# Kernel tuning notes

Measured on AMD Instinct MI355X. Metric: run time of the kernel, lower is better.

The kernel has to match this reference:

```python
import jax, jax.numpy as jnp
import numpy as np

# DeformConv3d hyperparams (from init_kwargs)
STRIDE = (1, 1, 1)
PAD = (1, 1, 1)
DIL = (1, 1, 1)
GROUPS = 1
DEFORM_GROUPS = 1  # reference assumes dg == 1


def setup_inputs() -> dict:
    key = jax.random.key(0)
    k1, k2, k3, k4 = jax.random.split(key, 4)
    x = jax.random.normal(k1, (2, 32, 24, 24, 24), jnp.float32)
    # offset channels = 3 * dg * kD*kH*kW = 81, layout [k_idx, (dz,dy,dx)]
    offset = jax.random.normal(k2, (2, 81, 24, 24, 24), jnp.float32)
    weight = jax.random.normal(k3, (64, 32, 3, 3, 3), jnp.float32) * 0.05
    bias = jax.random.normal(k4, (64,), jnp.float32) * 0.05
    return {"x": x, "offset": offset, "weight": weight, "bias": bias}


def _deform_conv3d(x, offset, weight, bias):
    B, C, D, H, W = x.shape
    Cout, Cg, kD, kH, kW = weight.shape
    sD, sH, sW = STRIDE
    pD, pH, pW = PAD
    dD, dH, dW = DIL
    Kn = kD * kH * kW
    Do = (D + 2 * pD - dD * (kD - 1) - 1) // sD + 1
    Ho = (H + 2 * pH - dH * (kH - 1) - 1) // sH + 1
    Wo = (W + 2 * pW - dW * (kW - 1) - 1) // sW + 1
    N = Do * Ho * Wo

    # offset: [B, Kn*3, Do,Ho,Wo] -> [B, Kn, 3, N]
    off = offset.reshape(B, Kn, 3, N)

    # kernel tap grid [Kn]
    kz, ky, kx = jnp.meshgrid(jnp.arange(kD), jnp.arange(kH), jnp.arange(kW), indexing='ij')
    kz, ky, kx = kz.reshape(Kn), ky.reshape(Kn), kx.reshape(Kn)
    # output grid [N]
    oz, oy, ox = jnp.meshgrid(jnp.arange(Do), jnp.arange(Ho), jnp.arange(Wo), indexing='ij')
    oz, oy, ox = oz.reshape(N), oy.reshape(N), ox.reshape(N)

    # sampling coords [B, Kn, N]
    z = (oz[None, None, :] * sD - pD) + kz[None, :, None] * dD + off[:, :, 0]
    y = (oy[None, None, :] * sH - pH) + ky[None, :, None] * dH + off[:, :, 1]
    xx = (ox[None, None, :] * sW - pW) + kx[None, :, None] * dW + off[:, :, 2]

    z0 = jnp.floor(z); fz = z - z0
    y0 = jnp.floor(y); fy = y - y0
    x0 = jnp.floor(xx); fx = xx - x0

    x_flat = x.reshape(B, C, D * H * W)
    acc = jnp.zeros((B, C, Kn * N), x.dtype)
    # 8 trilinear corners (fixed small loop)
    for dz in (0, 1):
        iz = z0 + dz
        wz = fz if dz else (1.0 - fz)
        for dy in (0, 1):
            iy = y0 + dy
            wy = fy if dy else (1.0 - fy)
            for dx in (0, 1):
                ix = x0 + dx
                wx = fx if dx else (1.0 - fx)
                valid = ((iz >= 0) & (iz < D) & (iy >= 0) & (iy < H)
                         & (ix >= 0) & (ix < W))
                w = (wz * wy * wx) * valid.astype(x.dtype)  # [B,Kn,N]
                izc = jnp.clip(iz, 0, D - 1).astype(jnp.int32)
                iyc = jnp.clip(iy, 0, H - 1).astype(jnp.int32)
                ixc = jnp.clip(ix, 0, W - 1).astype(jnp.int32)
                idx = (izc * H + iyc) * W + ixc  # [B,Kn,N]
                g = jnp.take_along_axis(x_flat, idx.reshape(B, 1, Kn * N), axis=2)
                acc = acc + g * w.reshape(B, 1, Kn * N)

    # im2col columns ordered (c, kz, ky, kx) to match weight layout
    cols = acc.reshape(B, C * Kn, N)
    Cpg = C // GROUPS
    Opg = Cout // GROUPS
    cols_g = cols.reshape(B, GROUPS, Cpg * Kn, N)
    w_g = weight.reshape(GROUPS, Opg, Cpg * Kn)
    out = jnp.einsum('gok,bgkn->bgon', w_g, cols_g).reshape(B, Cout, N)
    out = out + bias[None, :, None]
    return out.reshape(B, Cout, Do, Ho, Wo)


def reference(x, offset, weight, bias):
    return _deform_conv3d(x, offset, weight, bias)
```

## Files before the change

kernel.cpp:

```cpp
#include <hip/hip_runtime.h>
#include <hip/hip_fp16.h>


constexpr int B   = 2;
constexpr int C   = 32;
constexpr int D   = 24, H = 24, W = 24;
constexpr int CO  = 64;
constexpr int KN  = 27;
constexpr int DHW = D * H * W;
constexpr int N   = DHW;
constexpr int CK  = C * KN;

constexpr int NPOS     = 32;
constexpr int NTAP     = NPOS * KN;
constexpr int NTASK    = NTAP * 4;
constexpr int TPB_MAIN = 576;
constexpr int PADR     = CK + 8;
constexpr int NBLK     = (B * N) / NPOS;

constexpr int PREPX_BLKS = (B * DHW) / 256;
constexpr int PREPW_BLKS = (CO * CK) / 256;

using h8v   = __attribute__((ext_vector_type(8))) _Float16;
using f32x4 = __attribute__((ext_vector_type(4))) float;

__device__ __forceinline__ h8v splat8(float w) {
    const _Float16 h = (_Float16)w;
    h8v r;
    #pragma unroll
    for (int i = 0; i < 8; ++i) r[i] = h;
    return r;
}

__device__ __forceinline__ unsigned pack2h(float a, float b) {
    const _Float16 ha = (_Float16)a, hb = (_Float16)b;
    unsigned short ua, ub;
    __builtin_memcpy(&ua, &ha, 2);
    __builtin_memcpy(&ub, &hb, 2);
    return (unsigned)ua | ((unsigned)ub << 16);
}

__global__ __launch_bounds__(256)
void prep_fused(const float* __restrict__ x, const float* __restrict__ wgt,
                _Float16* __restrict__ xT, _Float16* __restrict__ wp) {
    const int bid = blockIdx.x;
    if (bid < PREPX_BLKS) {
        __shared__ unsigned s_t[256 * 21];
        const int tid = threadIdx.x;
        const int v0  = bid * 256;
        const int b   = (v0 >= DHW) ? 1 : 0;
        const int vox = (v0 - b * DHW) + tid;
        const float* xb = x + (size_t)(b * C) * DHW + vox;
        #pragma unroll
        for (int c2 = 0; c2 < 16; ++c2) {
            const float f0 = xb[(size_t)(2 * c2)     * DHW];
            const float f1 = xb[(size_t)(2 * c2 + 1) * DHW];
            s_t[tid * 21 + c2] = pack2h(f0, f1);
        }
        __syncthreads();
        unsigned r[16];
        #pragma unroll
        for (int j = 0; j < 16; ++j) r[j] = s_t[tid * 21 + j];
        int4* dst = reinterpret_cast<int4*>(xT + ((size_t)(v0 + tid)) * 32);
        dst[0] = make_int4(r[0],  r[1],  r[2],  r[3]);
        dst[1] = make_int4(r[4],  r[5],  r[6],  r[7]);
        dst[2] = make_int4(r[8],  r[9],  r[10], r[11]);
        dst[3] = make_int4(r[12], r[13], r[14], r[15]);
    } else {
        const int idx   = (bid - PREPX_BLKS) * 256 + threadIdx.x;
        const int j     = idx & 7;
        const int lane  = (idx >> 3) & 63;
        const int t     = idx >> 9;
        const int otile = t / 27;
        const int kstep = t - otile * 27;
        const int o     = otile * 16 + (lane & 15);
        const int c     = 8 * (lane >> 4) + j;
        wp[idx] = (_Float16)wgt[(size_t)o * CK + c * KN + kstep];
    }
}

__global__ __launch_bounds__(TPB_MAIN, 5)
void deform_main(const float* __restrict__ off,
                 const _Float16* __restrict__ xT,
                 const _Float16* __restrict__ wp,
                 const float* __restrict__ bias,
                 float* __restrict__ out) {
    __shared__ _Float16 s_vb[NPOS * PADR];

    const int tid   = threadIdx.x;
    const int blk   = blockIdx.x;
    const int n0    = blk * NPOS;
    const int b     = n0 / N;
    const int nbase = n0 - b * N;
    const h8v* xbase = reinterpret_cast<const h8v*>(xT) + (size_t)b * DHW * 4;
    const float* offb = off + (size_t)(b * 81) * N;

    #pragma unroll 1
    for (int r = 0; r < 6; ++r) {
        const int tau = tid + r * TPB_MAIN;
        const int q   = tau & 3;
        const int tap = tau >> 2;
        const int p   = tap & 31;
        const int k   = tap >> 5;
        const int n   = nbase + p;
        const int oz = n / 576;
        const int rr = n - oz * 576;
        const int oy = rr / 24;
        const int ox = rr - oy * 24;
        const int kz = k / 9;
        const int kr = k - kz * 9;
        const int ky = kr / 3;
        const int kx = kr - ky * 3;

        const float offz = offb[((size_t)(k * 3 + 0)) * N + n];
        const float offy = offb[((size_t)(k * 3 + 1)) * N + n];
        const float offx = offb[((size_t)(k * 3 + 2)) * N + n];

        const float z  = (float)(oz - 1 + kz) + offz;
        const float y  = (float)(oy - 1 + ky) + offy;
        const float xx = (float)(ox - 1 + kx) + offx;
        const float zf = floorf(z), yf = floorf(y), xf = floorf(xx);
        const float fz = z - zf, fy = y - yf, fx = xx - xf;
        const int z0 = (int)zf, y0 = (int)yf, x0 = (int)xf;

        int   cidx[8];
        float cw[8];
        #pragma unroll
        for (int cr = 0; cr < 8; ++cr) {
            const int cz = cr >> 2, cy = (cr >> 1) & 1, cx = cr & 1;
            const int iz = z0 + cz, iy = y0 + cy, ix = x0 + cx;
            const bool vd = ((unsigned)iz < (unsigned)D) &&
                            ((unsigned)iy < (unsigned)H) &&
                            ((unsigned)ix < (unsigned)W);
            const int izc = min(max(iz, 0), D - 1);
            const int iyc = min(max(iy, 0), H - 1);
            const int ixc = min(max(ix, 0), W - 1);
            cidx[cr] = (izc * H + iyc) * W + ixc;
            const float wz = cz ? fz : 1.0f - fz;
            const float wy = cy ? fy : 1.0f - fy;
            const float wx = cx ? fx : 1.0f - fx;
            cw[cr] = vd ? (wz * wy * wx) : 0.0f;
        }

        h8v v[8];
        #pragma unroll
        for (int cr = 0; cr < 8; ++cr)
            v[cr] = xbase[(size_t)cidx[cr] * 4 + q];
        h8v acc = splat8(0.0f);
        #pragma unroll
        for (int cr = 0; cr < 8; ++cr)
            acc += v[cr] * splat8(cw[cr]);

        *reinterpret_cast<h8v*>(&s_vb[p * PADR + k * 32 + q * 8]) = acc;
    }
    __syncthreads();

    const int wv = tid >> 6;
    if (wv < 8) {
        const int lane = tid & 63;
        const int ot   = wv & 3;
        const int pt   = wv >> 2;
        const int p    = pt * 16 + (lane & 15);
        f32x4 acc4 = {0.f, 0.f, 0.f, 0.f};
        const h8v* wrow = reinterpret_cast<const h8v*>(wp) + (ot * 27) * 64 + lane;
        const int lrow = p * PADR;
        const int lcol = (lane >> 4) * 8;
        #pragma unroll
        for (int ks = 0; ks < 27; ++ks) {
            const h8v a  = wrow[ks * 64];
            const h8v bf = *reinterpret_cast<const h8v*>(&s_vb[lrow + ks * 32 + lcol]);
            acc4 = __builtin_amdgcn_mfma_f32_16x16x32_f16(a, bf, acc4, 0, 0, 0);
        }
        const int n = nbase + p;
        const int obase = ot * 16 + (lane >> 4) * 4;
        #pragma unroll
        for (int rr = 0; rr < 4; ++rr) {
            const int o = obase + rr;
            out[((size_t)(b * CO + o)) * N + n] = acc4[rr] + bias[o];
        }
    }
}

extern "C" void kernel_launch(void* const* d_in, const int* in_sizes, int n_in,
                              void* d_out, int out_size, void* d_ws, size_t ws_size,
                              hipStream_t stream) {
    const float* x    = (const float*)d_in[0];
    const float* off  = (const float*)d_in[1];
    const float* wgt  = (const float*)d_in[2];
    const float* bias = (const float*)d_in[3];
    float* out = (float*)d_out;

    _Float16* xT = (_Float16*)d_ws;
    _Float16* wp = (_Float16*)((char*)d_ws + 1769472);

    prep_fused<<<PREPX_BLKS + PREPW_BLKS, 256, 0, stream>>>(x, wgt, xT, wp);
    deform_main<<<NBLK, TPB_MAIN, 0, stream>>>(off, xT, wp, bias, out);
}
```

Before: 100.1 us.

## Fuse trilinear gather directly into MFMA fragments, removing LDS staging

Each wave now owns 16 output positions and, for each of the 27 taps, builds the B fragment for the MFMA in registers from the trilinear gather, then multiplies it against four weight tiles covering all 64 output channels. This removes the shared-memory im2col buffer, the block barrier, and the idle waves in the GEMM phase, and raises occupancy by dropping LDS use. In exchange, every wave reloads weight fragments from global memory for each tap, and the gather for a position is done by 4 lanes per wave instead of being spread over a larger block.

```diff
diff --git a/kernel.cpp b/kernel.cpp
--- a/kernel.cpp
+++ b/kernel.cpp
@@ -11,12 +11,8 @@
 constexpr int N   = DHW;
 constexpr int CK  = C * KN;
 
-constexpr int NPOS     = 32;
-constexpr int NTAP     = NPOS * KN;
-constexpr int NTASK    = NTAP * 4;
-constexpr int TPB_MAIN = 576;
-constexpr int PADR     = CK + 8;
-constexpr int NBLK     = (B * N) / NPOS;
+constexpr int TPB_MAIN = 256;
+constexpr int NBLK     = (B * N) / 64;
 
 constexpr int PREPX_BLKS = (B * DHW) / 256;
 constexpr int PREPW_BLKS = (CO * CK) / 256;
@@ -79,42 +75,49 @@
     }
 }
 
-__global__ __launch_bounds__(TPB_MAIN, 5)
+__global__ __launch_bounds__(TPB_MAIN)
 void deform_main(const float* __restrict__ off,
                  const _Float16* __restrict__ xT,
                  const _Float16* __restrict__ wp,
                  const float* __restrict__ bias,
                  float* __restrict__ out) {
-    __shared__ _Float16 s_vb[NPOS * PADR];
+    const int tid  = threadIdx.x;
+    const int lane = tid & 63;
+    const int wv   = tid >> 6;
+    const int p    = lane & 15;
+    const int q    = lane >> 4;
 
-    const int tid   = threadIdx.x;
-    const int blk   = blockIdx.x;
-    const int n0    = blk * NPOS;
-    const int b     = n0 / N;
-    const int nbase = n0 - b * N;
-    const h8v* xbase = reinterpret_cast<const h8v*>(xT) + (size_t)b * DHW * 4;
-    const float* offb = off + (size_t)(b * 81) * N;
+    const int gp = blockIdx.x * 64 + wv * 16 + p;
+    const int b  = (gp >= N) ? 1 : 0;
+    const int n  = gp - b * N;
+    const int oz = n / 576;
+    const int rr = n - oz * 576;
+    const int oy = rr / 24;
+    const int ox = rr - oy * 24;
+
+    const float* offb  = off + (size_t)(b * 81) * N + n;
+    const h8v*   xbase = reinterpret_cast<const h8v*>(xT) + (size_t)b * DHW * 4;
+    const h8v*   wbase = reinterpret_cast<const h8v*>(wp);
+
+    f32x4 acc[4];
+    #pragma unroll
+    for (int ot = 0; ot < 4; ++ot) acc[ot] = (f32x4){0.f, 0.f, 0.f, 0.f};
 
     #pragma unroll 1
-    for (int r = 0; r < 6; ++r) {
-        const int tau = tid + r * TPB_MAIN;
-        const int q   = tau & 3;
-        const int tap = tau >> 2;
-        const int p   = tap & 31;
-        const int k   = tap >> 5;
-        const int n   = nbase + p;
-        const int oz = n / 576;
-        const int rr = n - oz * 576;
-        const int oy = rr / 24;
-        const int ox = rr - oy * 24;
-        const int kz = k / 9;
-        const int kr = k - kz * 9;
+    for (int ks = 0; ks < KN; ++ks) {
+        const int kz = ks / 9;
+        const int kr = ks - kz * 9;
         const int ky = kr / 3;
         const int kx = kr - ky * 3;
 
-        const float offz = offb[((size_t)(k * 3 + 0)) * N + n];
-        const float offy = offb[((size_t)(k * 3 + 1)) * N + n];
-        const float offx = offb[((size_t)(k * 3 + 2)) * N + n];
+        const float offz = offb[(size_t)(ks * 3 + 0) * N];
+        const float offy = offb[(size_t)(ks * 3 + 1) * N];
+        const float offx = offb[(size_t)(ks * 3 + 2) * N];
+
+        h8v afr[4];
+        #pragma unroll
+        for (int ot = 0; ot < 4; ++ot)
+            afr[ot] = wbase[(ot * 27 + ks) * 64 + lane];
 
         const float z  = (float)(oz - 1 + kz) + offz;
         const float y  = (float)(oy - 1 + ky) + offy;
@@ -146,37 +149,24 @@
         #pragma unroll
         for (int cr = 0; cr < 8; ++cr)
             v[cr] = xbase[(size_t)cidx[cr] * 4 + q];
-        h8v acc = splat8(0.0f);
+
+        h8v bfr = splat8(0.0f);
         #pragma unroll
         for (int cr = 0; cr < 8; ++cr)
-            acc += v[cr] * splat8(cw[cr]);
+            bfr += v[cr] * splat8(cw[cr]);
 
-        *reinterpret_cast<h8v*>(&s_vb[p * PADR + k * 32 + q * 8]) = acc;
+        #pragma unroll
+        for (int ot = 0; ot < 4; ++ot)
+            acc[ot] = __builtin_amdgcn_mfma_f32_16x16x32_f16(afr[ot], bfr,
+                                                             acc[ot], 0, 0, 0);
     }
-    __syncthreads();
 
-    const int wv = tid >> 6;
-    if (wv < 8) {
-        const int lane = tid & 63;
-        const int ot   = wv & 3;
-        const int pt   = wv >> 2;
-        const int p    = pt * 16 + (lane & 15);
-        f32x4 acc4 = {0.f, 0.f, 0.f, 0.f};
-        const h8v* wrow = reinterpret_cast<const h8v*>(wp) + (ot * 27) * 64 + lane;
-        const int lrow = p * PADR;
-        const int lcol = (lane >> 4) * 8;
+    #pragma unroll
+    for (int ot = 0; ot < 4; ++ot) {
         #pragma unroll
-        for (int ks = 0; ks < 27; ++ks) {
-            const h8v a  = wrow[ks * 64];
-            const h8v bf = *reinterpret_cast<const h8v*>(&s_vb[lrow + ks * 32 + lcol]);
-            acc4 = __builtin_amdgcn_mfma_f32_16x16x32_f16(a, bf, acc4, 0, 0, 0);
-        }
-        const int n = nbase + p;
-        const int obase = ot * 16 + (lane >> 4) * 4;
-        #pragma unroll
-        for (int rr = 0; rr < 4; ++rr) {
-            const int o = obase + rr;
-            out[((size_t)(b * CO + o)) * N + n] = acc4[rr] + bias[o];
+        for (int r = 0; r < 4; ++r) {
+            const int o = ot * 16 + q * 4 + r;
+            out[((size_t)(b * CO + o)) * N + n] = acc[ot][r] + bias[o];
         }
     }
 }
```

Measured after the change: 111.7 us. +11.6%, slower.
